# Performance work log

Hardware: AMD Instinct MI355X
Metric: run time of the kernel (lower is better)

The kernel has to match this reference:

```python
import jax, jax.numpy as jnp
import numpy as np

B, L, D = 2, 2048, 1024
H = 16
DH = D // H
DFF = 4096
THETA = 10000.0
EPS = 1e-5


def setup_inputs() -> dict:
    key = jax.random.key(0)
    ks = jax.random.split(key, 6)
    s_qkv = (2.0 / (D + 3 * D)) ** 0.5
    s_o = (2.0 / (D + D)) ** 0.5
    s_ff = (2.0 / (D + DFF)) ** 0.5
    return {
        'x': jax.random.normal(ks[0], (B, L, D), jnp.float32),
        'w_qkv': jax.random.normal(ks[1], (3 * D, D), jnp.float32) * s_qkv,
        'w_o': jax.random.normal(ks[2], (D, D), jnp.float32) * s_o,
        'w1': jax.random.normal(ks[3], (DFF, D), jnp.float32) * s_ff,
        'w2': jax.random.normal(ks[4], (D, DFF), jnp.float32) * s_ff,
        'w3': jax.random.normal(ks[5], (DFF, D), jnp.float32) * s_ff,
        'g1': jnp.ones((D,), jnp.float32),
        'g2': jnp.ones((D,), jnp.float32),
    }


def _rmsnorm(x, g):
    xf = x.astype(jnp.float32)
    inv = jax.lax.rsqrt(jnp.mean(xf * xf, axis=-1, keepdims=True) + EPS)
    return (xf * inv * g).astype(x.dtype)


def _rotate_pair(t):
    # interleaved pairs: (x0,x1,x2,x3,...) -> (-x1,x0,-x3,x2,...)
    t2 = t.reshape(t.shape[:-1] + (t.shape[-1] // 2, 2))
    r = jnp.stack((-t2[..., 1], t2[..., 0]), axis=-1)
    return r.reshape(t.shape)


def reference(x, w_qkv, w_o, w1, w2, w3, g1, g2):
    Bb, Ll, Dd = x.shape
    # --- attention sublayer ---
    y = _rmsnorm(x, g1)
    qkv = y @ w_qkv.T                       # (B, L, 3D)
    q, k, v = jnp.split(qkv, 3, axis=-1)
    def to_heads(t):
        return t.reshape(Bb, Ll, H, DH).transpose(0, 2, 1, 3)  # (B,H,L,Dh)
    q, k, v = to_heads(q), to_heads(k), to_heads(v)
    # RoPE (interleaved), positions = 0..L-1
    inv_freq = 1.0 / (THETA ** (jnp.arange(0, DH, 2, dtype=jnp.float32) / DH))
    ang = jnp.arange(Ll, dtype=jnp.float32)[:, None] * inv_freq  # (L, Dh/2)
    ang = jnp.repeat(ang, 2, axis=-1)                            # (L, Dh)
    cos, sin = jnp.cos(ang), jnp.sin(ang)
    q = q * cos + _rotate_pair(q) * sin
    k = k * cos + _rotate_pair(k) * sin
    att = jnp.einsum('bhqd,bhkd->bhqk', q, k) * (1.0 / np.sqrt(DH))
    causal = jnp.tril(jnp.ones((Ll, Ll), dtype=bool))
    att = jnp.where(causal, att, -jnp.inf)
    att = jax.nn.softmax(att, axis=-1)
    yh = jnp.einsum('bhqk,bhkd->bhqd', att, v)
    y = yh.transpose(0, 2, 1, 3).reshape(Bb, Ll, Dd)
    x = x + y @ w_o.T
    # --- SwiGLU FFN sublayer ---
    y = _rmsnorm(x, g2)
    h = jax.nn.silu(y @ w1.T) * (y @ w3.T)
    return x + h @ w2.T
```

## Files before the change

### kernel.cpp

```cpp
#include <hip/hip_runtime.h>


typedef __attribute__((ext_vector_type(8))) short short8;
typedef __attribute__((ext_vector_type(4))) float f32x4;

#define DEV __device__ __forceinline__

DEV unsigned short f2b(float f) {
  unsigned int u = __builtin_bit_cast(unsigned int, f);
  unsigned int r = u + 0x7fffu + ((u >> 16) & 1u);
  return (unsigned short)(r >> 16);
}
DEV float b2f(unsigned short h) {
  return __builtin_bit_cast(float, ((unsigned int)h) << 16);
}
DEV unsigned int cvtpk(float lo, float hi) {
  unsigned int r;
  asm("v_cvt_pk_bf16_f32 %0, %1, %2" : "=v"(r) : "v"(lo), "v"(hi));
  return r;
}
DEV f32x4 MFMA(short8 a, short8 b, f32x4 c) {
  return __builtin_amdgcn_mfma_f32_16x16x32_bf16(a, b, c, 0, 0, 0);
}
DEV void gload16(const void* g, void* lds) {
  __builtin_amdgcn_global_load_lds((const __attribute__((address_space(1))) void*)g,
                                   (__attribute__((address_space(3))) void*)lds, 16, 0, 0);
}

__global__ __launch_bounds__(256) void prep_k(
    const float* __restrict__ wqkv, const float* __restrict__ wo,
    const float* __restrict__ w1, const float* __restrict__ w3,
    const float* __restrict__ w2,
    unsigned short* __restrict__ wqkv_b, unsigned short* __restrict__ wo_b,
    unsigned short* __restrict__ w1_b, unsigned short* __restrict__ w3_b,
    unsigned short* __restrict__ w2_b,
    float2* __restrict__ rtab,
    const float* __restrict__ x, const float* __restrict__ g1,
    unsigned short* __restrict__ yb) {
  const int bid = blockIdx.x;
  const int t = threadIdx.x;
  if (bid < 16384) {
    const float* src;
    unsigned short* dst;
    int base;
    if (bid < 3072) { src = wqkv; dst = wqkv_b; base = bid; }
    else if (bid < 4096) { src = wo; dst = wo_b; base = bid - 3072; }
    else if (bid < 8192) { src = w1; dst = w1_b; base = bid - 4096; }
    else if (bid < 12288) { src = w3; dst = w3_b; base = bid - 8192; }
    else { src = w2; dst = w2_b; base = bid - 12288; }
    const int i = (base * 256 + t) * 4;
    float4 v = *(const float4*)(src + i);
    ushort4 o;
    o.x = f2b(v.x); o.y = f2b(v.y); o.z = f2b(v.z); o.w = f2b(v.w);
    *(ushort4*)(dst + i) = o;
  } else if (bid < 16640) {
    const int i = (bid - 16384) * 256 + t;
    const int lt = i >> 5, pr = i & 31;
    const float invf = __expf((float)pr * -0.28782313662425572f);
    const float ang = (float)lt * invf;
    float sn, cs;
    sincosf(ang, &sn, &cs);
    rtab[i] = make_float2(cs, sn);
  } else {
    const int row = bid - 16640;
    const float4 v = *(const float4*)(x + (size_t)row * 1024 + t * 4);
    float ss = v.x * v.x + v.y * v.y + v.z * v.z + v.w * v.w;
#pragma unroll
    for (int m = 32; m >= 1; m >>= 1) ss += __shfl_xor(ss, m, 64);
    __shared__ float red[4];
    if ((t & 63) == 0) red[t >> 6] = ss;
    __syncthreads();
    float tot = red[0] + red[1] + red[2] + red[3];
    float inv = rsqrtf(tot * (1.0f / 1024.0f) + 1e-5f);
    ushort4 o;
    o.x = f2b(v.x * inv * g1[t * 4 + 0]);
    o.y = f2b(v.y * inv * g1[t * 4 + 1]);
    o.z = f2b(v.z * inv * g1[t * 4 + 2]);
    o.w = f2b(v.w * inv * g1[t * 4 + 3]);
    *(ushort4*)(yb + (size_t)row * 1024 + t * 4) = o;
  }
}

__global__ __launch_bounds__(256) void rms_k(const float* __restrict__ x,
                                             const float* __restrict__ g,
                                             unsigned short* __restrict__ out) {
  const int row = blockIdx.x;
  const int t = threadIdx.x;
  const float4 v = *(const float4*)(x + (size_t)row * 1024 + t * 4);
  float ss = v.x * v.x + v.y * v.y + v.z * v.z + v.w * v.w;
#pragma unroll
  for (int m = 32; m >= 1; m >>= 1) ss += __shfl_xor(ss, m, 64);
  __shared__ float red[4];
  if ((t & 63) == 0) red[t >> 6] = ss;
  __syncthreads();
  float tot = red[0] + red[1] + red[2] + red[3];
  float inv = rsqrtf(tot * (1.0f / 1024.0f) + 1e-5f);
  ushort4 o;
  o.x = f2b(v.x * inv * g[t * 4 + 0]);
  o.y = f2b(v.y * inv * g[t * 4 + 1]);
  o.z = f2b(v.z * inv * g[t * 4 + 2]);
  o.w = f2b(v.w * inv * g[t * 4 + 3]);
  *(ushort4*)(out + (size_t)row * 1024 + t * 4) = o;
}

template <int MODE>
__global__ __launch_bounds__(256, 3) void gemm_bt(
    const unsigned short* __restrict__ A, const unsigned short* __restrict__ B0,
    int M, int N, int K,
    float* __restrict__ outF, const float* __restrict__ resid,
    unsigned short* __restrict__ q, unsigned short* __restrict__ k2,
    unsigned short* __restrict__ v,
    const float2* __restrict__ rtab) {
  __shared__ __align__(16) unsigned short As[2][128 * 32];
  __shared__ __align__(16) unsigned short Bs[2][128 * 32];
  const int t = threadIdx.x;
  const int wv = t >> 6, ln = t & 63;
  const int l15 = ln & 15, grp = ln >> 4;
  const int wr = wv >> 1, wc = wv & 1;
  int m0, n0;
  if constexpr (MODE == 1) {
    const int d = blockIdx.y * 8 + blockIdx.x;
    const int xcd = d & 7, j = d >> 3;
    m0 = (xcd * 4 + (j >> 3)) * 128;
    n0 = (j & 7) * 128;
  } else {
    const int d = blockIdx.x;
    const int xcd = d & 7, qd = d >> 3;
    m0 = (xcd + 8 * (qd / 24)) * 128;
    n0 = (qd % 24) * 128;
  }

  const char* sA0 = (const char*)A + ((size_t)(m0 + (t >> 2)) * K + (t & 3) * 8) * 2;
  const char* sA1 = (const char*)A + ((size_t)(m0 + 64 + (t >> 2)) * K + (t & 3) * 8) * 2;
  const char* sB0 = (const char*)B0 + ((size_t)(n0 + (t >> 2)) * K + (t & 3) * 8) * 2;
  const char* sB1 = (const char*)B0 + ((size_t)(n0 + 64 + (t >> 2)) * K + (t & 3) * 8) * 2;

  f32x4 acc[4][4];
#pragma unroll
  for (int mm = 0; mm < 4; ++mm)
#pragma unroll
    for (int nn = 0; nn < 4; ++nn) acc[mm][nn] = (f32x4){0.f, 0.f, 0.f, 0.f};

  const int KT = K >> 5;
  gload16(sA0, (char*)As[0] + wv * 1024);
  gload16(sA1, (char*)As[0] + 4096 + wv * 1024);
  gload16(sB0, (char*)Bs[0] + wv * 1024);
  gload16(sB1, (char*)Bs[0] + 4096 + wv * 1024);

#pragma unroll 1
  for (int kt = 0; kt < KT; ++kt) {
    const int par = kt & 1;
    const size_t ko = (size_t)((kt + 1 < KT) ? (kt + 1) : kt) * 64;
    gload16(sA0 + ko, (char*)As[par ^ 1] + wv * 1024);
    gload16(sA1 + ko, (char*)As[par ^ 1] + 4096 + wv * 1024);
    gload16(sB0 + ko, (char*)Bs[par ^ 1] + wv * 1024);
    gload16(sB1 + ko, (char*)Bs[par ^ 1] + 4096 + wv * 1024);
    asm volatile("s_waitcnt vmcnt(4)" ::: "memory");
    __builtin_amdgcn_s_barrier();
    const unsigned short* Ab = As[par];
    const unsigned short* Bb = Bs[par];
    short8 af[4], bf0[4];
#pragma unroll
    for (int mm = 0; mm < 4; ++mm)
      af[mm] = *(const short8*)&Ab[(wr * 64 + mm * 16 + l15) * 32 + grp * 8];
#pragma unroll
    for (int nn = 0; nn < 4; ++nn)
      bf0[nn] = *(const short8*)&Bb[(wc * 64 + nn * 16 + l15) * 32 + grp * 8];
#pragma unroll
    for (int mm = 0; mm < 4; ++mm)
#pragma unroll
      for (int nn = 0; nn < 4; ++nn) acc[mm][nn] = MFMA(af[mm], bf0[nn], acc[mm][nn]);
    __builtin_amdgcn_s_barrier();
  }

#pragma unroll
  for (int mm = 0; mm < 4; ++mm)
#pragma unroll
    for (int nn = 0; nn < 4; ++nn)
#pragma unroll
      for (int j = 0; j < 4; ++j) {
        const int r = m0 + wr * 64 + mm * 16 + grp * 4 + j;
        const int c = n0 + wc * 64 + nn * 16 + l15;
        float val = acc[mm][nn][j];
        if constexpr (MODE == 0) {
          const int mat = c >> 10;
          const int rem = c & 1023;
          const int hh = rem >> 6;
          const int dh = rem & 63;
          const int bt = r >> 11;
          const int lt = r & 2047;
          float outv = val;
          if (mat < 2) {
            const float partner = __shfl_xor(val, 1, 64);
            const float2 cs = rtab[lt * 32 + (dh >> 1)];
            outv = (dh & 1) ? (val * cs.x + partner * cs.y) : (val * cs.x - partner * cs.y);
          }
          if (mat == 0) outv *= 0.18033688011112042f;
          unsigned short* dst = (mat == 0) ? q : ((mat == 1) ? k2 : v);
          dst[((size_t)(bt * 16 + hh) * 2048 + lt) * 64 + dh] = f2b(outv);
        } else {
          const size_t idx = (size_t)r * N + c;
          outF[idx] = resid[idx] + val;
        }
      }
}

__global__ __launch_bounds__(256, 3) void gemm_sk(
    const unsigned short* __restrict__ A, const unsigned short* __restrict__ B0,
    unsigned short* __restrict__ part) {
  __shared__ __align__(16) unsigned short As[2][128 * 32];
  __shared__ __align__(16) unsigned short Bs[2][128 * 32];
  const int t = threadIdx.x;
  const int wv = t >> 6, ln = t & 63;
  const int l15 = ln & 15, grp = ln >> 4;
  const int wr = wv >> 1, wc = wv & 1;
  const int d = blockIdx.y * 8 + blockIdx.x;
  const int xcd = d & 7, j = d >> 3;
  const int m0 = (xcd * 4 + (j >> 3)) * 128;
  const int n0 = (j & 7) * 128;
  const size_t kbase = (size_t)blockIdx.z * 2048;

  const char* sA0 = (const char*)A + ((size_t)(m0 + (t >> 2)) * 4096 + kbase + (t & 3) * 8) * 2;
  const char* sA1 = (const char*)A + ((size_t)(m0 + 64 + (t >> 2)) * 4096 + kbase + (t & 3) * 8) * 2;
  const char* sB0 = (const char*)B0 + ((size_t)(n0 + (t >> 2)) * 4096 + kbase + (t & 3) * 8) * 2;
  const char* sB1 = (const char*)B0 + ((size_t)(n0 + 64 + (t >> 2)) * 4096 + kbase + (t & 3) * 8) * 2;

  f32x4 acc[4][4];
#pragma unroll
  for (int mm = 0; mm < 4; ++mm)
#pragma unroll
    for (int nn = 0; nn < 4; ++nn) acc[mm][nn] = (f32x4){0.f, 0.f, 0.f, 0.f};

  gload16(sA0, (char*)As[0] + wv * 1024);
  gload16(sA1, (char*)As[0] + 4096 + wv * 1024);
  gload16(sB0, (char*)Bs[0] + wv * 1024);
  gload16(sB1, (char*)Bs[0] + 4096 + wv * 1024);

#pragma unroll 1
  for (int kt = 0; kt < 64; ++kt) {
    const int par = kt & 1;
    const size_t ko = (size_t)((kt + 1 < 64) ? (kt + 1) : kt) * 64;
    gload16(sA0 + ko, (char*)As[par ^ 1] + wv * 1024);
    gload16(sA1 + ko, (char*)As[par ^ 1] + 4096 + wv * 1024);
    gload16(sB0 + ko, (char*)Bs[par ^ 1] + wv * 1024);
    gload16(sB1 + ko, (char*)Bs[par ^ 1] + 4096 + wv * 1024);
    asm volatile("s_waitcnt vmcnt(4)" ::: "memory");
    __builtin_amdgcn_s_barrier();
    const unsigned short* Ab = As[par];
    const unsigned short* Bb = Bs[par];
    short8 af[4], bf0[4];
#pragma unroll
    for (int mm = 0; mm < 4; ++mm)
      af[mm] = *(const short8*)&Ab[(wr * 64 + mm * 16 + l15) * 32 + grp * 8];
#pragma unroll
    for (int nn = 0; nn < 4; ++nn)
      bf0[nn] = *(const short8*)&Bb[(wc * 64 + nn * 16 + l15) * 32 + grp * 8];
#pragma unroll
    for (int mm = 0; mm < 4; ++mm)
#pragma unroll
      for (int nn = 0; nn < 4; ++nn) acc[mm][nn] = MFMA(af[mm], bf0[nn], acc[mm][nn]);
    __builtin_amdgcn_s_barrier();
  }

  unsigned short* pz = part + (size_t)blockIdx.z * 4194304;
#pragma unroll
  for (int mm = 0; mm < 4; ++mm)
#pragma unroll
    for (int nn = 0; nn < 4; ++nn)
#pragma unroll
      for (int j = 0; j < 4; ++j) {
        const int r = m0 + wr * 64 + mm * 16 + grp * 4 + j;
        const int c = n0 + wc * 64 + nn * 16 + l15;
        pz[(size_t)r * 1024 + c] = f2b(acc[mm][nn][j]);
      }
}

__global__ __launch_bounds__(256) void red_k(const float* __restrict__ x2,
                                             const unsigned short* __restrict__ part,
                                             float* __restrict__ out) {
  const int i = (blockIdx.x * 256 + threadIdx.x) * 4;
  float4 r = *(const float4*)(x2 + i);
#pragma unroll
  for (int z = 0; z < 2; ++z) {
    const ushort4 p = *(const ushort4*)(part + (size_t)z * 4194304 + i);
    r.x += b2f(p.x);
    r.y += b2f(p.y);
    r.z += b2f(p.z);
    r.w += b2f(p.w);
  }
  *(float4*)(out + i) = r;
}

__global__ __launch_bounds__(512, 2) void ffn_k(
    const unsigned short* __restrict__ A, const unsigned short* __restrict__ B0,
    const unsigned short* __restrict__ B1, unsigned short* __restrict__ outH) {
  __shared__ __align__(16) char Asm[2][32768];
  __shared__ __align__(16) char Bsm[2][32768];
  const int t = threadIdx.x;
  const int wid = t >> 6, lane = t & 63;
  const int l15 = lane & 15, grp = lane >> 4;
  const int wr = wid >> 2, wc = wid & 3;
  const int d = blockIdx.x;
  const int xcd = d & 7, r8 = d >> 3;
  const int m0 = (r8 >> 2) * 256;
  const int n0 = (xcd * 4 + (r8 & 3)) * 256;

  const char* srcA0;
  const char* srcB0;
  {
    const int lb = t * 16;
    const int r = lb >> 7;
    const int sw = (((lb >> 4) & 7) * 16) ^ ((r & 7) << 4);
    srcA0 = (const char*)A + (size_t)(m0 + r) * 2048 + sw;
    const int R = n0 + r;
    const unsigned short* bsrc = ((R >> 4) & 1) ? B1 : B0;
    const int br = ((R >> 5) << 4) + (R & 15);
    srcB0 = (const char*)bsrc + (size_t)br * 2048 + sw;
  }
  char* const ldsA = (char*)Asm + wid * 1024;
  char* const ldsB = (char*)Bsm + wid * 1024;

  f32x4 acc[8][4];
#pragma unroll
  for (int m = 0; m < 8; ++m)
#pragma unroll
    for (int n = 0; n < 4; ++n) acc[m][n] = (f32x4){0.f, 0.f, 0.f, 0.f};

  gload16(srcA0 + 0 * 131072, ldsA + 0 * 8192);
  gload16(srcA0 + 1 * 131072, ldsA + 1 * 8192);
  gload16(srcB0 + 0 * 65536, ldsB + 0 * 8192);
  gload16(srcB0 + 1 * 65536, ldsB + 1 * 8192);
  gload16(srcB0 + 2 * 65536, ldsB + 2 * 8192);
  gload16(srcB0 + 3 * 65536, ldsB + 3 * 8192);
  gload16(srcA0 + 2 * 131072, ldsA + 2 * 8192);
  gload16(srcA0 + 3 * 131072, ldsA + 3 * 8192);

  const int rA0 = wr * 64 + l15;
  const int rB0 = wc * 32 + l15;

#pragma unroll 1
  for (int kt = 0; kt < 16; ++kt) {
    const int cb = kt & 1;
    const size_t koff = (size_t)((kt + 1 < 16) ? (kt + 1) : kt) * 128;
    const char* Ab = Asm[cb];
    const char* Bb = Bsm[cb];
    const int nb = (cb ^ 1) * 32768;

    short8 a0[2][4], a1[2][4], b0[2][2], b1[2][2];

    gload16(srcA0 + 0 * 131072 + koff, ldsA + nb + 0 * 8192);
    gload16(srcA0 + 1 * 131072 + koff, ldsA + nb + 1 * 8192);
    asm volatile("s_waitcnt vmcnt(4)" ::: "memory");
    __builtin_amdgcn_s_barrier();
#pragma unroll
    for (int ks = 0; ks < 2; ++ks)
#pragma unroll
      for (int m = 0; m < 4; ++m) {
        const int r = rA0 + m * 16;
        a0[ks][m] = *(const short8*)(Ab + r * 128 + ((ks * 64 + grp * 16) ^ ((r & 7) << 4)));
      }
#pragma unroll
    for (int ks = 0; ks < 2; ++ks)
#pragma unroll
      for (int n = 0; n < 2; ++n) {
        const int r = rB0 + n * 16;
        b0[ks][n] = *(const short8*)(Bb + r * 128 + ((ks * 64 + grp * 16) ^ ((r & 7) << 4)));
      }
#pragma unroll
    for (int ks = 0; ks < 2; ++ks)
#pragma unroll
      for (int n = 0; n < 2; ++n) {
        const int r = 128 + rB0 + n * 16;
        b1[ks][n] = *(const short8*)(Bb + r * 128 + ((ks * 64 + grp * 16) ^ ((r & 7) << 4)));
      }
    __builtin_amdgcn_s_setprio(1);
#pragma unroll
    for (int ks = 0; ks < 2; ++ks)
#pragma unroll
      for (int m = 0; m < 4; ++m)
#pragma unroll
        for (int n = 0; n < 2; ++n) acc[m][n] = MFMA(a0[ks][m], b0[ks][n], acc[m][n]);
    __builtin_amdgcn_s_setprio(0);

    gload16(srcB0 + 0 * 65536 + koff, ldsB + nb + 0 * 8192);
    gload16(srcB0 + 1 * 65536 + koff, ldsB + nb + 1 * 8192);
    gload16(srcB0 + 2 * 65536 + koff, ldsB + nb + 2 * 8192);
    gload16(srcB0 + 3 * 65536 + koff, ldsB + nb + 3 * 8192);
    asm volatile("s_waitcnt vmcnt(6)" ::: "memory");
    __builtin_amdgcn_s_barrier();
#pragma unroll
    for (int ks = 0; ks < 2; ++ks)
#pragma unroll
      for (int m = 0; m < 4; ++m) {
        const int r = 128 + rA0 + m * 16;
        a1[ks][m] = *(const short8*)(Ab + r * 128 + ((ks * 64 + grp * 16) ^ ((r & 7) << 4)));
      }
    __builtin_amdgcn_s_setprio(1);
#pragma unroll
    for (int ks = 0; ks < 2; ++ks)
#pragma unroll
      for (int m = 0; m < 4; ++m)
#pragma unroll
        for (int n = 0; n < 2; ++n) acc[m][2 + n] = MFMA(a0[ks][m], b1[ks][n], acc[m][2 + n]);
    __builtin_amdgcn_s_setprio(0);

    gload16(srcA0 + 2 * 131072 + koff, ldsA + nb + 2 * 8192);
    gload16(srcA0 + 3 * 131072 + koff, ldsA + nb + 3 * 8192);
    __builtin_amdgcn_s_barrier();
    __builtin_amdgcn_s_setprio(1);
#pragma unroll
    for (int ks = 0; ks < 2; ++ks)
#pragma unroll
      for (int m = 0; m < 4; ++m)
#pragma unroll
        for (int n = 0; n < 2; ++n) acc[4 + m][2 + n] = MFMA(a1[ks][m], b1[ks][n], acc[4 + m][2 + n]);
    __builtin_amdgcn_s_setprio(0);

    __builtin_amdgcn_s_barrier();
    __builtin_amdgcn_s_setprio(1);
#pragma unroll
    for (int ks = 0; ks < 2; ++ks)
#pragma unroll
      for (int m = 0; m < 4; ++m)
#pragma unroll
        for (int n = 0; n < 2; ++n) acc[4 + m][n] = MFMA(a1[ks][m], b0[ks][n], acc[4 + m][n]);
    __builtin_amdgcn_s_setprio(0);
  }

#pragma unroll
  for (int mh = 0; mh < 2; ++mh)
#pragma unroll
    for (int m = 0; m < 4; ++m)
#pragma unroll
      for (int nh = 0; nh < 2; ++nh)
#pragma unroll
        for (int j = 0; j < 4; ++j) {
          const int row = m0 + mh * 128 + wr * 64 + m * 16 + grp * 4 + j;
          const int ch = (n0 >> 1) + nh * 64 + wc * 16 + l15;
          const float a1v = acc[mh * 4 + m][nh * 2 + 0][j];
          const float a3v = acc[mh * 4 + m][nh * 2 + 1][j];
          const float hval = a1v / (1.0f + __expf(-a1v)) * a3v;
          outH[(size_t)row * 4096 + ch] = f2b(hval);
        }
}

__global__ __launch_bounds__(256) void vtr_k(const unsigned short* __restrict__ v,
                                             unsigned short* __restrict__ vt) {
  __shared__ __align__(16) unsigned short tile[64][72];
  const int bh = blockIdx.y;
  const int lt0 = blockIdx.x * 64;
  const int t = threadIdx.x;
  const int r = t >> 2;
  const int c0 = (t & 3) * 16;
  const unsigned short* src = v + ((size_t)bh * 2048 + lt0 + r) * 64 + c0;
  *(short8*)&tile[r][c0] = *(const short8*)src;
  *(short8*)&tile[r][c0 + 8] = *(const short8*)(src + 8);
  __syncthreads();
  unsigned short outv[16];
#pragma unroll
  for (int i = 0; i < 16; ++i) outv[i] = tile[c0 + i][r];
  unsigned short* dst = vt + ((size_t)bh * 64 + r) * 2048 + lt0 + c0;
  *(short8*)dst = *(short8*)&outv[0];
  *(short8*)(dst + 8) = *(short8*)&outv[8];
}

__global__ __launch_bounds__(256) void attn_k(const unsigned short* __restrict__ qb,
                                              const unsigned short* __restrict__ kb,
                                              const unsigned short* __restrict__ vt,
                                              unsigned short* __restrict__ yh) {
  const int dd = blockIdx.x;
  const int xcd = dd & 7, idx = dd >> 3;
  const int bh = xcd + 8 * (idx & 3);
  const int pair = idx >> 2;
  const int t = threadIdx.x;
  const int w = t >> 6, lane = t & 63;
  const int l15 = lane & 15, grp = lane >> 4;

  __shared__ __align__(16) char Ks[2][16384];
  __shared__ __align__(16) char Vs[2][16384];
  __shared__ __align__(16) char Ps[16384];
  char* Pw = Ps + w * 4096;

  const char* kg = (const char*)kb + (size_t)bh * 262144;
  const char* vg = (const char*)vt + (size_t)bh * 262144;

  const char* srcK[4];
  const char* srcV[4];
#pragma unroll
  for (int s = 0; s < 4; ++s) {
    const int lb = s * 4096 + t * 16;
    const int rK = lb >> 7;
    const int oK = (lb & 0x70) ^ ((rK & 7) << 4);
    srcK[s] = kg + rK * 128 + oK;
    const int rV = lb >> 8;
    const int oV = (lb & 0xF0) ^ ((rV & 7) << 4);
    srcV[s] = vg + (size_t)rV * 4096 + oV;
  }

  const int bq = bh >> 4, hh = bh & 15;

#pragma unroll 1
  for (int half = 0; half < 2; ++half) {
    const int qblk = half ? pair : (31 - pair);
    const int qw = qblk * 64 + w * 16;

    const unsigned short* qp = qb + ((size_t)bh * 2048 + qw) * 64;
    const short8 qf0 = *(const short8*)(qp + l15 * 64 + grp * 8);
    const short8 qf1 = *(const short8*)(qp + l15 * 64 + 32 + grp * 8);

    f32x4 o[4];
#pragma unroll
    for (int d = 0; d < 4; ++d) o[d] = (f32x4){0.f, 0.f, 0.f, 0.f};
    float mrun = -3.0e38f, lrun = 0.f;

    const int nkt = (qblk + 2) >> 1;

    __syncthreads();
#pragma unroll
    for (int s = 0; s < 4; ++s) {
      gload16(srcK[s], Ks[0] + s * 4096 + w * 1024);
      gload16(srcV[s], Vs[0] + s * 4096 + w * 1024);
    }

#pragma unroll 1
    for (int kt = 0; kt < nkt; ++kt) {
      const int par = kt & 1;
      const int ktn = (kt + 1 < nkt) ? (kt + 1) : kt;
#pragma unroll
      for (int s = 0; s < 4; ++s) {
        gload16(srcK[s] + (size_t)ktn * 16384, Ks[par ^ 1] + s * 4096 + w * 1024);
        gload16(srcV[s] + (size_t)ktn * 256, Vs[par ^ 1] + s * 4096 + w * 1024);
      }
      asm volatile("s_waitcnt vmcnt(8)" ::: "memory");
      __builtin_amdgcn_s_barrier();

      const char* Kc = Ks[par];
      const char* Vc = Vs[par];

      f32x4 st[8];
#pragma unroll
      for (int c = 0; c < 8; ++c) {
        const int r = c * 16 + l15;
        const int xr = (r & 7) << 4;
        const short8 kf0 = *(const short8*)(Kc + r * 128 + ((grp * 16) ^ xr));
        const short8 kf1 = *(const short8*)(Kc + r * 128 + ((64 + grp * 16) ^ xr));
        f32x4 z = (f32x4){0.f, 0.f, 0.f, 0.f};
        __builtin_amdgcn_s_setprio(1);
        z = MFMA(kf0, qf0, z);
        z = MFMA(kf1, qf1, z);
        __builtin_amdgcn_s_setprio(0);
        st[c] = z;
      }

      const bool diag = (kt * 128 + 127 > qw);
      const int qg = qw + l15;
      float tm = -3.0e38f;
#pragma unroll
      for (int c = 0; c < 8; ++c)
#pragma unroll
        for (int j = 0; j < 4; ++j) {
          float x = st[c][j];
          if (diag) {
            const int kg2 = kt * 128 + c * 16 + grp * 4 + j;
            if (kg2 > qg) x = -3.0e38f;
          }
          st[c][j] = x;
          tm = fmaxf(tm, x);
        }
      tm = fmaxf(tm, __shfl_xor(tm, 16, 64));
      tm = fmaxf(tm, __shfl_xor(tm, 32, 64));

      const float mold = mrun;
      const bool need = tm > mold;
      mrun = fmaxf(mold, tm);
      const float aown = need ? __builtin_amdgcn_exp2f(mold - mrun) : 1.0f;
      if (__any(need)) {
        float am[4];
#pragma unroll
        for (int j = 0; j < 4; ++j) am[j] = __shfl(aown, grp * 4 + j, 64);
#pragma unroll
        for (int d = 0; d < 4; ++d)
#pragma unroll
          for (int j = 0; j < 4; ++j) o[d][j] *= am[j];
      }

      float rs = 0.f;
      uint2 pk[8];
#pragma unroll
      for (int c = 0; c < 8; ++c) {
        const float p0 = __builtin_amdgcn_exp2f(st[c][0] - mrun);
        const float p1 = __builtin_amdgcn_exp2f(st[c][1] - mrun);
        const float p2 = __builtin_amdgcn_exp2f(st[c][2] - mrun);
        const float p3 = __builtin_amdgcn_exp2f(st[c][3] - mrun);
        rs += (p0 + p1) + (p2 + p3);
        pk[c].x = cvtpk(p0, p1);
        pk[c].y = cvtpk(p2, p3);
      }
      rs += __shfl_xor(rs, 16, 64);
      rs += __shfl_xor(rs, 32, 64);
      lrun = lrun * aown + rs;

      const int xp = (l15 & 7) << 4;
      char* prow = Pw + l15 * 256;
#pragma unroll
      for (int c = 0; c < 8; ++c)
        *(uint2*)(prow + ((32 * c + 8 * grp) ^ xp)) = pk[c];

      short8 pa[4];
#pragma unroll
      for (int ks = 0; ks < 4; ++ks)
        pa[ks] = *(const short8*)(prow + ((ks * 64 + grp * 16) ^ xp));
#pragma unroll
      for (int db = 0; db < 4; ++db) {
        const int rv = db * 16 + l15;
        const int xv = (rv & 7) << 4;
        __builtin_amdgcn_s_setprio(1);
#pragma unroll
        for (int ks = 0; ks < 4; ++ks) {
          const short8 vf = *(const short8*)(Vc + rv * 256 + ((ks * 64 + grp * 16) ^ xv));
          o[db] = MFMA(pa[ks], vf, o[db]);
        }
        __builtin_amdgcn_s_setprio(0);
      }
      __builtin_amdgcn_s_barrier();
    }

    float lr[4];
#pragma unroll
    for (int j = 0; j < 4; ++j) lr[j] = __shfl(lrun, grp * 4 + j, 64);
#pragma unroll
    for (int db = 0; db < 4; ++db)
#pragma unroll
      for (int j = 0; j < 4; ++j) {
        const float valo = o[db][j] / lr[j];
        const size_t rowo = (size_t)bq * 2048 + qw + grp * 4 + j;
        yh[rowo * 1024 + hh * 64 + db * 16 + l15] = f2b(valo);
      }
  }
}

extern "C" void kernel_launch(void* const* d_in, const int* in_sizes, int n_in,
                              void* d_out, int out_size, void* d_ws, size_t ws_size,
                              hipStream_t stream) {
  const float* x = (const float*)d_in[0];
  const float* wqkv = (const float*)d_in[1];
  const float* wo = (const float*)d_in[2];
  const float* w1 = (const float*)d_in[3];
  const float* w2 = (const float*)d_in[4];
  const float* w3 = (const float*)d_in[5];
  const float* g1 = (const float*)d_in[6];
  const float* g2 = (const float*)d_in[7];

  char* ws = (char*)d_ws;
  unsigned short* wqkv_b = (unsigned short*)(ws + 0);
  unsigned short* wo_b = (unsigned short*)(ws + 6291456);
  unsigned short* w1_b = (unsigned short*)(ws + 8388608);
  unsigned short* w3_b = (unsigned short*)(ws + 16777216);
  unsigned short* yb = (unsigned short*)(ws + 25165824);
  float* x2 = (float*)(ws + 33554432);
  float2* rtab = (float2*)(ws + 33554432);
  unsigned short* w2_b = (unsigned short*)(ws + 50331648);
  unsigned short* qb = (unsigned short*)(ws + 58720256);
  unsigned short* kb = (unsigned short*)(ws + 67108864);
  unsigned short* vb = (unsigned short*)(ws + 75497472);
  unsigned short* vt = (unsigned short*)(ws + 83886080);
  unsigned short* yh = vb;
  unsigned short* hb = (unsigned short*)(ws + 58720256);
  unsigned short* part = (unsigned short*)(ws + 0);
  if (ws_size < 92274688) return;

  prep_k<<<20736, 256, 0, stream>>>(wqkv, wo, w1, w3, w2,
                                    wqkv_b, wo_b, w1_b, w3_b, w2_b,
                                    rtab, x, g1, yb);
  gemm_bt<0><<<dim3(768), 256, 0, stream>>>(yb, wqkv_b, 4096, 3072, 1024,
                                            nullptr, nullptr, qb, kb, vb, rtab);
  vtr_k<<<dim3(32, 32), 256, 0, stream>>>(vb, vt);
  attn_k<<<dim3(512), 256, 0, stream>>>(qb, kb, vt, yh);
  gemm_bt<1><<<dim3(8, 32), 256, 0, stream>>>(yh, wo_b, 4096, 1024, 1024,
                                              x2, x, nullptr, nullptr, nullptr, nullptr);
  rms_k<<<4096, 256, 0, stream>>>(x2, g2, yb);
  ffn_k<<<dim3(512), 512, 0, stream>>>(yb, w1_b, w3_b, hb);
  gemm_sk<<<dim3(8, 32, 2), 256, 0, stream>>>(hb, w2_b, part);
  red_k<<<4096, 256, 0, stream>>>(x2, part, (float*)d_out);
}
```

Baseline: 267.5 us.

## Use 1024-thread blocks in FFN GEMM with smaller per-wave tiles

The fused SwiGLU up-projection kernel now launches 16 waves per block instead of 8. Each wave owns a 64x64 output tile, so it holds 16 accumulators instead of 32, and the phased four-quadrant schedule becomes a simple double-buffered loop. All loads for the next k-tile are issued up front, followed by one barrier per stage. The aim is to cut register pressure and raise the wave count available to hide latency. The cost is more LDS fragment reads per MFMA and less overlap between loads and compute inside each iteration.

Result: no change. 271.7 us (+1.6%).

```diff
diff --git a/kernel.cpp b/kernel.cpp
--- a/kernel.cpp
+++ b/kernel.cpp
@@ -291,7 +291,7 @@
   *(float4*)(out + i) = r;
 }
 
-__global__ __launch_bounds__(512, 2) void ffn_k(
+__global__ __launch_bounds__(1024) void ffn_k(
     const unsigned short* __restrict__ A, const unsigned short* __restrict__ B0,
     const unsigned short* __restrict__ B1, unsigned short* __restrict__ outH) {
   __shared__ __align__(16) char Asm[2][32768];
@@ -310,7 +310,7 @@
   {
     const int lb = t * 16;
     const int r = lb >> 7;
-    const int sw = (((lb >> 4) & 7) * 16) ^ ((r & 7) << 4);
+    const int sw = (lb & 0x70) ^ ((r & 7) << 4);
     srcA0 = (const char*)A + (size_t)(m0 + r) * 2048 + sw;
     const int R = n0 + r;
     const unsigned short* bsrc = ((R >> 4) & 1) ? B1 : B0;
@@ -320,128 +320,69 @@
   char* const ldsA = (char*)Asm + wid * 1024;
   char* const ldsB = (char*)Bsm + wid * 1024;
 
-  f32x4 acc[8][4];
-#pragma unroll
-  for (int m = 0; m < 8; ++m)
+  f32x4 acc[4][4];
+#pragma unroll
+  for (int m = 0; m < 4; ++m)
 #pragma unroll
     for (int n = 0; n < 4; ++n) acc[m][n] = (f32x4){0.f, 0.f, 0.f, 0.f};
 
-  gload16(srcA0 + 0 * 131072, ldsA + 0 * 8192);
-  gload16(srcA0 + 1 * 131072, ldsA + 1 * 8192);
-  gload16(srcB0 + 0 * 65536, ldsB + 0 * 8192);
-  gload16(srcB0 + 1 * 65536, ldsB + 1 * 8192);
-  gload16(srcB0 + 2 * 65536, ldsB + 2 * 8192);
-  gload16(srcB0 + 3 * 65536, ldsB + 3 * 8192);
-  gload16(srcA0 + 2 * 131072, ldsA + 2 * 8192);
-  gload16(srcA0 + 3 * 131072, ldsA + 3 * 8192);
+  gload16(srcA0, ldsA + 0 * 16384);
+  gload16(srcA0 + 262144, ldsA + 1 * 16384);
+  gload16(srcB0, ldsB + 0 * 16384);
+  gload16(srcB0 + 131072, ldsB + 1 * 16384);
 
   const int rA0 = wr * 64 + l15;
-  const int rB0 = wc * 32 + l15;
+  const int rB0 = wc * 64 + l15;
 
 #pragma unroll 1
   for (int kt = 0; kt < 16; ++kt) {
-    const int cb = kt & 1;
-    const size_t koff = (size_t)((kt + 1 < 16) ? (kt + 1) : kt) * 128;
-    const char* Ab = Asm[cb];
-    const char* Bb = Bsm[cb];
-    const int nb = (cb ^ 1) * 32768;
-
-    short8 a0[2][4], a1[2][4], b0[2][2], b1[2][2];
-
-    gload16(srcA0 + 0 * 131072 + koff, ldsA + nb + 0 * 8192);
-    gload16(srcA0 + 1 * 131072 + koff, ldsA + nb + 1 * 8192);
+    const int par = kt & 1;
+    const size_t ko = (size_t)((kt + 1 < 16) ? (kt + 1) : kt) * 128;
+    const int nb = (par ^ 1) * 32768;
+    gload16(srcA0 + ko, ldsA + nb + 0 * 16384);
+    gload16(srcA0 + 262144 + ko, ldsA + nb + 1 * 16384);
+    gload16(srcB0 + ko, ldsB + nb + 0 * 16384);
+    gload16(srcB0 + 131072 + ko, ldsB + nb + 1 * 16384);
     asm volatile("s_waitcnt vmcnt(4)" ::: "memory");
     __builtin_amdgcn_s_barrier();
-#pragma unroll
-    for (int ks = 0; ks < 2; ++ks)
+    const char* Ab = Asm[par];
+    const char* Bb = Bsm[par];
+#pragma unroll
+    for (int ks = 0; ks < 2; ++ks) {
+      short8 af[4], bf[4];
 #pragma unroll
       for (int m = 0; m < 4; ++m) {
         const int r = rA0 + m * 16;
-        a0[ks][m] = *(const short8*)(Ab + r * 128 + ((ks * 64 + grp * 16) ^ ((r & 7) << 4)));
-      }
-#pragma unroll
-    for (int ks = 0; ks < 2; ++ks)
-#pragma unroll
-      for (int n = 0; n < 2; ++n) {
+        af[m] = *(const short8*)(Ab + r * 128 + ((ks * 64 + grp * 16) ^ ((r & 7) << 4)));
+      }
+#pragma unroll
+      for (int n = 0; n < 4; ++n) {
         const int r = rB0 + n * 16;
-        b0[ks][n] = *(const short8*)(Bb + r * 128 + ((ks * 64 + grp * 16) ^ ((r & 7) << 4)));
-      }
-#pragma unroll
-    for (int ks = 0; ks < 2; ++ks)
-#pragma unroll
-      for (int n = 0; n < 2; ++n) {
-        const int r = 128 + rB0 + n * 16;
-        b1[ks][n] = *(const short8*)(Bb + r * 128 + ((ks * 64 + grp * 16) ^ ((r & 7) << 4)));
-      }
-    __builtin_amdgcn_s_setprio(1);
-#pragma unroll
-    for (int ks = 0; ks < 2; ++ks)
+        bf[n] = *(const short8*)(Bb + r * 128 + ((ks * 64 + grp * 16) ^ ((r & 7) << 4)));
+      }
+      __builtin_amdgcn_s_setprio(1);
 #pragma unroll
       for (int m = 0; m < 4; ++m)
 #pragma unroll
-        for (int n = 0; n < 2; ++n) acc[m][n] = MFMA(a0[ks][m], b0[ks][n], acc[m][n]);
-    __builtin_amdgcn_s_setprio(0);
-
-    gload16(srcB0 + 0 * 65536 + koff, ldsB + nb + 0 * 8192);
-    gload16(srcB0 + 1 * 65536 + koff, ldsB + nb + 1 * 8192);
-    gload16(srcB0 + 2 * 65536 + koff, ldsB + nb + 2 * 8192);
-    gload16(srcB0 + 3 * 65536 + koff, ldsB + nb + 3 * 8192);
-    asm volatile("s_waitcnt vmcnt(6)" ::: "memory");
+        for (int n = 0; n < 4; ++n) acc[m][n] = MFMA(af[m], bf[n], acc[m][n]);
+      __builtin_amdgcn_s_setprio(0);
+    }
     __builtin_amdgcn_s_barrier();
-#pragma unroll
-    for (int ks = 0; ks < 2; ++ks)
-#pragma unroll
-      for (int m = 0; m < 4; ++m) {
-        const int r = 128 + rA0 + m * 16;
-        a1[ks][m] = *(const short8*)(Ab + r * 128 + ((ks * 64 + grp * 16) ^ ((r & 7) << 4)));
-      }
-    __builtin_amdgcn_s_setprio(1);
-#pragma unroll
-    for (int ks = 0; ks < 2; ++ks)
-#pragma unroll
-      for (int m = 0; m < 4; ++m)
-#pragma unroll
-        for (int n = 0; n < 2; ++n) acc[m][2 + n] = MFMA(a0[ks][m], b1[ks][n], acc[m][2 + n]);
-    __builtin_amdgcn_s_setprio(0);
-
-    gload16(srcA0 + 2 * 131072 + koff, ldsA + nb + 2 * 8192);
-    gload16(srcA0 + 3 * 131072 + koff, ldsA + nb + 3 * 8192);
-    __builtin_amdgcn_s_barrier();
-    __builtin_amdgcn_s_setprio(1);
-#pragma unroll
-    for (int ks = 0; ks < 2; ++ks)
-#pragma unroll
-      for (int m = 0; m < 4; ++m)
-#pragma unroll
-        for (int n = 0; n < 2; ++n) acc[4 + m][2 + n] = MFMA(a1[ks][m], b1[ks][n], acc[4 + m][2 + n]);
-    __builtin_amdgcn_s_setprio(0);
-
-    __builtin_amdgcn_s_barrier();
-    __builtin_amdgcn_s_setprio(1);
-#pragma unroll
-    for (int ks = 0; ks < 2; ++ks)
-#pragma unroll
-      for (int m = 0; m < 4; ++m)
-#pragma unroll
-        for (int n = 0; n < 2; ++n) acc[4 + m][n] = MFMA(a1[ks][m], b0[ks][n], acc[4 + m][n]);
-    __builtin_amdgcn_s_setprio(0);
-  }
-
-#pragma unroll
-  for (int mh = 0; mh < 2; ++mh)
-#pragma unroll
-    for (int m = 0; m < 4; ++m)
-#pragma unroll
-      for (int nh = 0; nh < 2; ++nh)
-#pragma unroll
-        for (int j = 0; j < 4; ++j) {
-          const int row = m0 + mh * 128 + wr * 64 + m * 16 + grp * 4 + j;
-          const int ch = (n0 >> 1) + nh * 64 + wc * 16 + l15;
-          const float a1v = acc[mh * 4 + m][nh * 2 + 0][j];
-          const float a3v = acc[mh * 4 + m][nh * 2 + 1][j];
-          const float hval = a1v / (1.0f + __expf(-a1v)) * a3v;
-          outH[(size_t)row * 4096 + ch] = f2b(hval);
-        }
+  }
+
+#pragma unroll
+  for (int m = 0; m < 4; ++m)
+#pragma unroll
+    for (int np = 0; np < 2; ++np)
+#pragma unroll
+      for (int j = 0; j < 4; ++j) {
+        const int row = m0 + wr * 64 + m * 16 + grp * 4 + j;
+        const int ch = (n0 >> 1) + wc * 32 + np * 16 + l15;
+        const float a1v = acc[m][2 * np][j];
+        const float a3v = acc[m][2 * np + 1][j];
+        const float hval = a1v / (1.0f + __expf(-a1v)) * a3v;
+        outH[(size_t)row * 4096 + ch] = f2b(hval);
+      }
 }
 
 __global__ __launch_bounds__(256) void vtr_k(const unsigned short* __restrict__ v,
@@ -679,7 +620,7 @@
   gemm_bt<1><<<dim3(8, 32), 256, 0, stream>>>(yh, wo_b, 4096, 1024, 1024,
                                               x2, x, nullptr, nullptr, nullptr, nullptr);
   rms_k<<<4096, 256, 0, stream>>>(x2, g2, yb);
-  ffn_k<<<dim3(512), 512, 0, stream>>>(yb, w1_b, w3_b, hb);
+  ffn_k<<<dim3(512), 1024, 0, stream>>>(yb, w1_b, w3_b, hb);
   gemm_sk<<<dim3(8, 32, 2), 256, 0, stream>>>(hb, w2_b, part);
   red_k<<<4096, 256, 0, stream>>>(x2, part, (float*)d_out);
 }
```
